# Performance work log

Hardware: AMD Instinct MI355X
Metric: run time of the kernel (lower is better)

## Reference

```python
import jax, jax.numpy as jnp
import numpy as np

# Model dims (DeepSeek-V2-Lite-like MLA)
B, S, DIM, H = 2, 2048, 2048, 16
QR, KVR = 1536, 512          # q_lora_rank, kv_lora_rank
DN, DR, DV = 128, 64, 128    # qk_nope_head_dim, qk_rope_head_dim, v_head_dim
QKD = DN + DR                # qk_head_dim = 192
SCALE = QKD ** -0.5          # max_seq_len == original_seq_len -> no mscale correction
EPS = float(jnp.finfo(jnp.float32).eps)  # torch.nn.RMSNorm default eps


def rmsnorm(x, w):
    return x * jax.lax.rsqrt(jnp.mean(x * x, axis=-1, keepdims=True) + EPS) * w


def rope(x, cos, sin):
    # x: [B, S, H, D]; cos/sin: [S, D//2]. Matches torch.view_as_complex on
    # consecutive (real, imag) pairs, multiply by freqs_cis, flatten back.
    xr, xi = x[..., 0::2], x[..., 1::2]
    c = cos[None, :, None, :]
    s = sin[None, :, None, :]
    yr = xr * c - xi * s
    yi = xr * s + xi * c
    return jnp.stack([yr, yi], axis=-1).reshape(x.shape)


def _xavier(key, out_f, in_f):
    lim = (6.0 / (in_f + out_f)) ** 0.5
    return jax.random.uniform(key, (out_f, in_f), jnp.float32, -lim, lim)


def setup_inputs() -> dict:
    key = jax.random.key(0)
    ks = jax.random.split(key, 8)
    x = jax.random.normal(ks[0], (B, S, DIM), jnp.float32)
    # rotary tables: theta=10000, rope dim = DR
    inv = 1.0 / (10000.0 ** (np.arange(0, DR, 2, dtype=np.float64) / DR))
    ang = np.arange(S, dtype=np.float64)[:, None] * inv[None, :]
    freqs_cos = jnp.asarray(np.cos(ang), jnp.float32)
    freqs_sin = jnp.asarray(np.sin(ang), jnp.float32)
    # causal mask [S, S]: 0 on/below diagonal, -1e9 above
    idx = jnp.arange(S)
    mask = jnp.where(idx[:, None] >= idx[None, :], 0.0, -1e9).astype(jnp.float32)
    return {
        "x": x,
        "freqs_cos": freqs_cos,
        "freqs_sin": freqs_sin,
        "mask": mask,
        "wq_a_w": _xavier(ks[1], QR, DIM), "wq_a_b": jnp.zeros((QR,), jnp.float32),
        "q_norm_w": jnp.ones((QR,), jnp.float32),
        "wq_b_w": _xavier(ks[2], H * QKD, QR), "wq_b_b": jnp.zeros((H * QKD,), jnp.float32),
        "wkv_a_w": _xavier(ks[3], KVR + DR, DIM), "wkv_a_b": jnp.zeros((KVR + DR,), jnp.float32),
        "kv_norm_w": jnp.ones((KVR,), jnp.float32),
        "wkv_b_w": _xavier(ks[4], H * (DN + DV), KVR), "wkv_b_b": jnp.zeros((H * (DN + DV),), jnp.float32),
        "wo_w": _xavier(ks[5], DIM, H * DV), "wo_b": jnp.zeros((DIM,), jnp.float32),
        "start_pos": 0,
    }


def reference(x, freqs_cos, freqs_sin, mask,
              wq_a_w, wq_a_b, q_norm_w, wq_b_w, wq_b_b,
              wkv_a_w, wkv_a_b, kv_norm_w, wkv_b_w, wkv_b_b,
              wo_w, wo_b, start_pos):
    bsz, seqlen, _ = x.shape
    # low-rank Q: wq_b(RMSNorm(wq_a(x)))
    q = rmsnorm(x @ wq_a_w.T + wq_a_b, q_norm_w) @ wq_b_w.T + wq_b_b
    q = q.reshape(bsz, seqlen, H, QKD)
    q_nope, q_pe = q[..., :DN], q[..., DN:]
    q_pe = rope(q_pe, freqs_cos, freqs_sin)
    # low-rank KV
    kv_a = x @ wkv_a_w.T + wkv_a_b               # [B,S,KVR+DR]
    kv_c, k_pe = kv_a[..., :KVR], kv_a[..., KVR:]
    k_pe = rope(k_pe[:, :, None, :], freqs_cos, freqs_sin)   # [B,S,1,DR]
    q = jnp.concatenate([q_nope, q_pe], axis=-1)             # [B,S,H,QKD]
    kv = rmsnorm(kv_c, kv_norm_w) @ wkv_b_w.T + wkv_b_b
    kv = kv.reshape(bsz, seqlen, H, DN + DV)
    k_nope, v = kv[..., :DN], kv[..., DN:]
    k = jnp.concatenate(
        [k_nope, jnp.broadcast_to(k_pe, (bsz, seqlen, H, DR))], axis=-1)
    scores = jnp.einsum('bshd,bthd->bsht', q, k) * SCALE
    scores = scores + mask[None, :, None, :]
    p = jax.nn.softmax(scores.astype(jnp.float32), axis=-1).astype(x.dtype)
    out = jnp.einsum('bsht,bthd->bshd', p, v).reshape(bsz, seqlen, H * DV)
    return out @ wo_w.T + wo_b
```

## Files before the change

kernel.cpp:

```cpp
#include <hip/hip_runtime.h>

#define SLEN 2048
#define NROW 4096
#define NH   16
#define SCALE_QK 0.07216878364870322f
#define RMS_EPS 1.1920928955078125e-07f

typedef __attribute__((ext_vector_type(8))) short bf16x8;
typedef __attribute__((ext_vector_type(4))) float f32x4;

__device__ __forceinline__ float b2f(short s) {
  union { float f; unsigned u; } x; x.u = ((unsigned)(unsigned short)s) << 16; return x.f;
}
__device__ __forceinline__ short f2b(float f) {
  union { float f; unsigned u; } x; x.f = f;
  unsigned r = x.u + 0x7FFFu + ((x.u >> 16) & 1u);
  return (short)(r >> 16);
}

#define GLOAD_LDS16(g, l) __builtin_amdgcn_global_load_lds( \
  (__attribute__((address_space(1))) void*)(g),             \
  (__attribute__((address_space(3))) void*)(l), 16, 0, 0)

__global__ __launch_bounds__(256) void f2b4_kernel(const float* __restrict__ in,
                                                   short* __restrict__ out, int n4) {
  int i = blockIdx.x * 256 + threadIdx.x;
  if (i >= n4) return;
  float4 v = ((const float4*)in)[i];
  short4 o = make_short4(f2b(v.x), f2b(v.y), f2b(v.z), f2b(v.w));
  ((short4*)out)[i] = o;
}

template<int OUT_BF16>
__global__ __launch_bounds__(256)
void gemm_bt_kernel(const short* __restrict__ A, const short* __restrict__ W,
                    const float* __restrict__ bias, void* __restrict__ Cout,
                    int M, int N, int K)
{
  __shared__ short sA[128 * 32];
  __shared__ short sB[128 * 32];
  int nbn = N >> 7;
  int nwg = gridDim.x;
  int wg = blockIdx.x;
  int cpx = nwg >> 3;
  wg = (wg & 7) * cpx + (wg >> 3);
  int bm = wg / nbn, bn = wg % nbn;
  int tid = threadIdx.x, wid = tid >> 6, lane = tid & 63;
  int wr = wid >> 1, wc = wid & 1;
  int lr = lane & 15, lg = lane >> 4;
  int srow = lane >> 2;
  int skk = (lane & 3) * 8;
  f32x4 acc[4][4] = {};
  const size_t baseA = (size_t)bm * 128 * K;
  const size_t baseW = (size_t)bn * 128 * K;

  for (int k0 = 0; k0 < K; k0 += 32) {
#pragma unroll
    for (int i = 0; i < 2; ++i) {
      int c = wid + i * 4;
      int r = c * 16 + srow;
      GLOAD_LDS16(A + baseA + (size_t)r * K + k0 + skk, &sA[c * 512]);
      GLOAD_LDS16(W + baseW + (size_t)r * K + k0 + skk, &sB[c * 512]);
    }
    asm volatile("s_waitcnt vmcnt(0)" ::: "memory");
    __syncthreads();
    bf16x8 av[4], bv[4];
#pragma unroll
    for (int m = 0; m < 4; ++m) av[m] = *(const bf16x8*)&sA[(wr * 64 + m * 16 + lr) * 32 + lg * 8];
#pragma unroll
    for (int n = 0; n < 4; ++n) bv[n] = *(const bf16x8*)&sB[(wc * 64 + n * 16 + lr) * 32 + lg * 8];
#pragma unroll
    for (int m = 0; m < 4; ++m)
#pragma unroll
      for (int n = 0; n < 4; ++n)
        acc[m][n] = __builtin_amdgcn_mfma_f32_16x16x32_bf16(av[m], bv[n], acc[m][n], 0, 0, 0);
    __syncthreads();
  }

  int row0 = bm * 128 + wr * 64, col0 = bn * 128 + wc * 64;
#pragma unroll
  for (int n = 0; n < 4; ++n) {
    int col = col0 + n * 16 + lr;
    float bb = bias[col];
#pragma unroll
    for (int m = 0; m < 4; ++m) {
#pragma unroll
      for (int j = 0; j < 4; ++j) {
        int row = row0 + m * 16 + lg * 4 + j;
        float v = acc[m][n][j] + bb;
        if (OUT_BF16) ((short*)Cout)[(size_t)row * N + col] = f2b(v);
        else          ((float*)Cout)[(size_t)row * N + col] = v;
      }
    }
  }
}

__global__ __launch_bounds__(256)
void norm_rope_kernel(const float* __restrict__ c1, const float* __restrict__ qw,
                      const float* __restrict__ kvw, const float* __restrict__ fcos,
                      const float* __restrict__ fsin, short* __restrict__ qan,
                      short* __restrict__ kvn, short* __restrict__ kpe)
{
  int row = blockIdx.x;
  int s = row & (SLEN - 1);
  const float* r = c1 + (size_t)row * 2176;
  int tid = threadIdx.x, wid = tid >> 6, lane = tid & 63;
  float vq[6], vk[2];
  float sq = 0.f, sk = 0.f;
#pragma unroll
  for (int i = 0; i < 6; ++i) { vq[i] = r[tid + i * 256]; sq += vq[i] * vq[i]; }
#pragma unroll
  for (int i = 0; i < 2; ++i) { vk[i] = r[1536 + tid + i * 256]; sk += vk[i] * vk[i]; }
#pragma unroll
  for (int off = 32; off > 0; off >>= 1) {
    sq += __shfl_xor(sq, off, 64);
    sk += __shfl_xor(sk, off, 64);
  }
  __shared__ float red[2][4];
  if (lane == 0) { red[0][wid] = sq; red[1][wid] = sk; }
  __syncthreads();
  sq = red[0][0] + red[0][1] + red[0][2] + red[0][3];
  sk = red[1][0] + red[1][1] + red[1][2] + red[1][3];
  float rq = rsqrtf(sq * (1.f / 1536.f) + RMS_EPS);
  float rk = rsqrtf(sk * (1.f / 512.f) + RMS_EPS);
#pragma unroll
  for (int i = 0; i < 6; ++i) qan[(size_t)row * 1536 + tid + i * 256] = f2b(vq[i] * rq * qw[tid + i * 256]);
#pragma unroll
  for (int i = 0; i < 2; ++i) kvn[(size_t)row * 512 + tid + i * 256] = f2b(vk[i] * rk * kvw[tid + i * 256]);
  if (tid < 32) {
    float xr = r[2048 + tid * 2], xi = r[2048 + tid * 2 + 1];
    float c = fcos[s * 32 + tid], sn = fsin[s * 32 + tid];
    kpe[(size_t)row * 64 + tid * 2]     = f2b(xr * c - xi * sn);
    kpe[(size_t)row * 64 + tid * 2 + 1] = f2b(xr * sn + xi * c);
  }
}

__global__ __launch_bounds__(256)
void rope_q_kernel(short* __restrict__ qf, const float* __restrict__ fcos,
                   const float* __restrict__ fsin)
{
  int idx = blockIdx.x * 256 + threadIdx.x;
  int pr = idx & 31; int h = (idx >> 5) & 15; int row = idx >> 9;
  int s = row & (SLEN - 1);
  short2* p = (short2*)(qf + (size_t)row * 3072 + h * 192 + 128 + pr * 2);
  short2 v = *p;
  float xr = b2f(v.x), xi = b2f(v.y);
  float c = fcos[s * 32 + pr], sn = fsin[s * 32 + pr];
  v.x = f2b(xr * c - xi * sn);
  v.y = f2b(xr * sn + xi * c);
  *p = v;
}

__device__ __forceinline__ void softmax16(f32x4* sacc, float p[4][4], float* m_i,
                                          float* l_i, f32x4* oacc, int t0, int srow0, int lr)
{
  float rmax[4];
#pragma unroll
  for (int j = 0; j < 4; ++j) rmax[j] = -1e30f;
#pragma unroll
  for (int tt = 0; tt < 4; ++tt) {
    int t = t0 + tt * 16 + lr;
#pragma unroll
    for (int j = 0; j < 4; ++j) {
      float x = sacc[tt][j] * SCALE_QK;
      if (t > srow0 + j) x = -1e30f;
      p[tt][j] = x;
      rmax[j] = fmaxf(rmax[j], x);
    }
  }
#pragma unroll
  for (int off = 1; off < 16; off <<= 1)
#pragma unroll
    for (int j = 0; j < 4; ++j) rmax[j] = fmaxf(rmax[j], __shfl_xor(rmax[j], off, 64));
  bool grow = false;
#pragma unroll
  for (int j = 0; j < 4; ++j) grow = grow || (rmax[j] > m_i[j] + 8.f);
  if (__any((int)grow)) {
    float sf[4];
#pragma unroll
    for (int j = 0; j < 4; ++j) {
      float mn = fmaxf(m_i[j], rmax[j]);
      sf[j] = __expf(m_i[j] - mn);
      m_i[j] = mn;
      l_i[j] *= sf[j];
    }
#pragma unroll
    for (int dt = 0; dt < 8; ++dt)
#pragma unroll
      for (int j = 0; j < 4; ++j) oacc[dt][j] *= sf[j];
  }
  float rsum[4] = {0.f, 0.f, 0.f, 0.f};
#pragma unroll
  for (int tt = 0; tt < 4; ++tt)
#pragma unroll
    for (int j = 0; j < 4; ++j) {
      float e = __expf(p[tt][j] - m_i[j]);
      p[tt][j] = e;
      rsum[j] += e;
    }
#pragma unroll
  for (int off = 1; off < 16; off <<= 1)
#pragma unroll
    for (int j = 0; j < 4; ++j) rsum[j] += __shfl_xor(rsum[j], off, 64);
#pragma unroll
  for (int j = 0; j < 4; ++j) l_i[j] += rsum[j];
}

__global__ __launch_bounds__(256, 2)
void attn_kernel(const short* __restrict__ qf, const short* __restrict__ kvf,
                 const short* __restrict__ kpe, short* __restrict__ obuf)
{
  __shared__ short sK[64 * 200];
  __shared__ short sVt[128 * 72];
  __shared__ short sPA[4][16 * 72];
  __shared__ short sPB[4][16 * 72];
  int bid = blockIdx.x;
  bid = (bid & 7) * 64 + (bid >> 3);
  int i = bid & 15, h = (bid >> 4) & 15, b = bid >> 8;
  int qtA = i, qtB = 31 - i;
  int base = b * SLEN;
  int tid = threadIdx.x, wid = tid >> 6, lane = tid & 63;
  int lr = lane & 15, lg = lane >> 4;
  int qrowA = base + qtA * 64 + wid * 16;
  int qrowB = base + qtB * 64 + wid * 16;

  bf16x8 qfragA[6], qfragB[6];
  {
    const short* qpA = qf + (size_t)(qrowA + lr) * 3072 + h * 192;
    const short* qpB = qf + (size_t)(qrowB + lr) * 3072 + h * 192;
#pragma unroll
    for (int kc = 0; kc < 6; ++kc) {
      qfragA[kc] = *(const bf16x8*)(qpA + kc * 32 + lg * 8);
      qfragB[kc] = *(const bf16x8*)(qpB + kc * 32 + lg * 8);
    }
  }
  f32x4 oaccA[8] = {}, oaccB[8] = {};
  float mA[4], lA[4], mB[4], lB[4];
#pragma unroll
  for (int j = 0; j < 4; ++j) { mA[j] = mB[j] = -1e30f; lA[j] = lB[j] = 0.f; }
  int srow0A = qtA * 64 + wid * 16 + lg * 4;
  int srow0B = qtB * 64 + wid * 16 + lg * 4;
  int str = tid >> 2, sp4 = tid & 3;
  int tpair = tid & 31, d0v = (tid >> 5) * 16;
  short* sPAw = sPA[wid];
  short* sPBw = sPB[wid];

  for (int it = 0; it <= qtB; ++it) {
    int t0 = it * 64;
    {
      const short* src = kvf + (size_t)(base + t0 + str) * 4096 + h * 256 + sp4 * 32;
      short* dst = &sK[str * 200 + sp4 * 32];
#pragma unroll
      for (int k = 0; k < 4; ++k) *(bf16x8*)(dst + k * 8) = *(const bf16x8*)(src + k * 8);
      const short* srcp = kpe + (size_t)(base + t0 + str) * 64 + sp4 * 16;
      short* dstp = &sK[str * 200 + 128 + sp4 * 16];
#pragma unroll
      for (int k = 0; k < 2; ++k) *(bf16x8*)(dstp + k * 8) = *(const bf16x8*)(srcp + k * 8);
      int tv = tpair * 2;
      const short* sv0 = kvf + (size_t)(base + t0 + tv) * 4096 + h * 256 + 128 + d0v;
      const short* sv1 = sv0 + 4096;
      bf16x8 va0 = *(const bf16x8*)(sv0);
      bf16x8 va1 = *(const bf16x8*)(sv0 + 8);
      bf16x8 vb0 = *(const bf16x8*)(sv1);
      bf16x8 vb1 = *(const bf16x8*)(sv1 + 8);
#pragma unroll
      for (int k = 0; k < 8; ++k) {
        unsigned w0 = (unsigned)(unsigned short)va0[k] | ((unsigned)(unsigned short)vb0[k] << 16);
        *((unsigned*)(sVt + (size_t)(d0v + k) * 72) + tpair) = w0;
        unsigned w1 = (unsigned)(unsigned short)va1[k] | ((unsigned)(unsigned short)vb1[k] << 16);
        *((unsigned*)(sVt + (size_t)(d0v + 8 + k) * 72) + tpair) = w1;
      }
    }
    __syncthreads();
    bool doA = (it <= qtA);

    f32x4 saccB[4] = {};
#pragma unroll
    for (int tt = 0; tt < 4; ++tt)
#pragma unroll
      for (int kc = 0; kc < 6; ++kc) {
        bf16x8 kf = *(const bf16x8*)&sK[(tt * 16 + lr) * 200 + kc * 32 + lg * 8];
        saccB[tt] = __builtin_amdgcn_mfma_f32_16x16x32_bf16(qfragB[kc], kf, saccB[tt], 0, 0, 0);
      }
    f32x4 saccA[4] = {};
    if (doA) {
#pragma unroll
      for (int tt = 0; tt < 4; ++tt)
#pragma unroll
        for (int kc = 0; kc < 6; ++kc) {
          bf16x8 kf = *(const bf16x8*)&sK[(tt * 16 + lr) * 200 + kc * 32 + lg * 8];
          saccA[tt] = __builtin_amdgcn_mfma_f32_16x16x32_bf16(qfragA[kc], kf, saccA[tt], 0, 0, 0);
        }
    }
    {
      float pB[4][4];
      softmax16(saccB, pB, mB, lB, oaccB, t0, srow0B, lr);
#pragma unroll
      for (int tt = 0; tt < 4; ++tt)
#pragma unroll
        for (int j = 0; j < 4; ++j)
          sPBw[(lg * 4 + j) * 72 + tt * 16 + lr] = f2b(pB[tt][j]);
    }
    if (doA) {
      float pA[4][4];
      softmax16(saccA, pA, mA, lA, oaccA, t0, srow0A, lr);
#pragma unroll
      for (int tt = 0; tt < 4; ++tt)
#pragma unroll
        for (int j = 0; j < 4; ++j)
          sPAw[(lg * 4 + j) * 72 + tt * 16 + lr] = f2b(pA[tt][j]);
    }
    asm volatile("s_waitcnt lgkmcnt(0)" ::: "memory");
    {
      bf16x8 pf[2];
#pragma unroll
      for (int kc = 0; kc < 2; ++kc) pf[kc] = *(const bf16x8*)&sPBw[lr * 72 + kc * 32 + lg * 8];
#pragma unroll
      for (int dt = 0; dt < 8; ++dt)
#pragma unroll
        for (int kc = 0; kc < 2; ++kc) {
          bf16x8 vf = *(const bf16x8*)&sVt[(dt * 16 + lr) * 72 + kc * 32 + lg * 8];
          oaccB[dt] = __builtin_amdgcn_mfma_f32_16x16x32_bf16(pf[kc], vf, oaccB[dt], 0, 0, 0);
        }
    }
    if (doA) {
      bf16x8 pf[2];
#pragma unroll
      for (int kc = 0; kc < 2; ++kc) pf[kc] = *(const bf16x8*)&sPAw[lr * 72 + kc * 32 + lg * 8];
#pragma unroll
      for (int dt = 0; dt < 8; ++dt)
#pragma unroll
        for (int kc = 0; kc < 2; ++kc) {
          bf16x8 vf = *(const bf16x8*)&sVt[(dt * 16 + lr) * 72 + kc * 32 + lg * 8];
          oaccA[dt] = __builtin_amdgcn_mfma_f32_16x16x32_bf16(pf[kc], vf, oaccA[dt], 0, 0, 0);
        }
    }
    __syncthreads();
  }

  float invA[4], invB[4];
#pragma unroll
  for (int j = 0; j < 4; ++j) { invA[j] = 1.f / lA[j]; invB[j] = 1.f / lB[j]; }
#pragma unroll
  for (int dt = 0; dt < 8; ++dt)
#pragma unroll
    for (int j = 0; j < 4; ++j) {
      int rowA = qrowA + lg * 4 + j;
      int rowB = qrowB + lg * 4 + j;
      obuf[(size_t)rowA * 2048 + h * 128 + dt * 16 + lr] = f2b(oaccA[dt][j] * invA[j]);
      obuf[(size_t)rowB * 2048 + h * 128 + dt * 16 + lr] = f2b(oaccB[dt][j] * invB[j]);
    }
}

extern "C" void kernel_launch(void* const* d_in, const int* in_sizes, int n_in,
                              void* d_out, int out_size, void* d_ws, size_t ws_size,
                              hipStream_t stream)
{
  const float* x    = (const float*)d_in[0];
  const float* fcos = (const float*)d_in[1];
  const float* fsin = (const float*)d_in[2];
  const float* wqa   = (const float*)d_in[4];
  const float* wqab  = (const float*)d_in[5];
  const float* qnw   = (const float*)d_in[6];
  const float* wqb   = (const float*)d_in[7];
  const float* wqbb  = (const float*)d_in[8];
  const float* wkva  = (const float*)d_in[9];
  const float* wkvab = (const float*)d_in[10];
  const float* kvnw  = (const float*)d_in[11];
  const float* wkvb  = (const float*)d_in[12];
  const float* wkvbb = (const float*)d_in[13];
  const float* wo    = (const float*)d_in[14];
  const float* wob   = (const float*)d_in[15];
  float* out = (float*)d_out;

  char* ws = (char*)d_ws;
  size_t off = 0;
  auto alloc = [&](size_t bytes) {
    char* p = ws + off;
    off += (bytes + 255) & ~(size_t)255;
    return p;
  };
  short* xb     = (short*)alloc(4096ull * 2048 * 2);
  short* w1     = (short*)alloc(2176ull * 2048 * 2);
  float* b1     = (float*)alloc(2176 * 4);
  short* wqb16  = (short*)alloc(3072ull * 1536 * 2);
  short* wkvb16 = (short*)alloc(4096ull * 512 * 2);
  short* wob16  = (short*)alloc(2048ull * 2048 * 2);
  float* c1     = (float*)alloc(4096ull * 2176 * 4);
  short* qan    = (short*)alloc(4096ull * 1536 * 2);
  short* kvn    = (short*)alloc(4096ull * 512 * 2);
  short* kpe    = (short*)alloc(4096ull * 64 * 2);
  short* qfull  = (short*)alloc(4096ull * 3072 * 2);
  short* kvfull = (short*)alloc(4096ull * 4096 * 2);
  short* obuf   = (short*)alloc(4096ull * 2048 * 2);
  (void)ws_size; (void)in_sizes; (void)n_in; (void)out_size;

  f2b4_kernel<<<8192, 256, 0, stream>>>(x, xb, 2097152);
  f2b4_kernel<<<3072, 256, 0, stream>>>(wqa, w1, 786432);
  f2b4_kernel<<<1152, 256, 0, stream>>>(wkva, w1 + 1536ull * 2048, 294912);
  hipMemsetAsync(w1 + 2112ull * 2048, 0, 64ull * 2048 * 2, stream);
  hipMemcpyAsync(b1, wqab, 1536 * 4, hipMemcpyDeviceToDevice, stream);
  hipMemcpyAsync(b1 + 1536, wkvab, 576 * 4, hipMemcpyDeviceToDevice, stream);
  hipMemsetAsync(b1 + 2112, 0, 64 * 4, stream);
  f2b4_kernel<<<4608, 256, 0, stream>>>(wqb, wqb16, 1179648);
  f2b4_kernel<<<2048, 256, 0, stream>>>(wkvb, wkvb16, 524288);
  f2b4_kernel<<<4096, 256, 0, stream>>>(wo, wob16, 1048576);

  gemm_bt_kernel<0><<<544, 256, 0, stream>>>(xb, w1, b1, c1, 4096, 2176, 2048);
  norm_rope_kernel<<<4096, 256, 0, stream>>>(c1, qnw, kvnw, fcos, fsin, qan, kvn, kpe);
  gemm_bt_kernel<1><<<768, 256, 0, stream>>>(qan, wqb16, wqbb, qfull, 4096, 3072, 1536);
  gemm_bt_kernel<1><<<1024, 256, 0, stream>>>(kvn, wkvb16, wkvbb, kvfull, 4096, 4096, 512);
  rope_q_kernel<<<8192, 256, 0, stream>>>(qfull, fcos, fsin);
  attn_kernel<<<512, 256, 0, stream>>>(qfull, kvfull, kpe, obuf);
  gemm_bt_kernel<0><<<512, 256, 0, stream>>>(obuf, wob16, wob, out, 4096, 2048, 2048);
}
```

Before: 563.6 us.

## Prefetch next K/V tile into registers, share P buffer, raise occupancy in attention

Restructures the attention loop so the next K/V tile's global loads are issued into registers after the QK MFMAs and written to LDS at the start of the next iteration, overlapping global latency with softmax and PV compute. The two per-wave P buffers are merged into one, with the key index permuted in both the P and V^T layouts so P can be stored as short4 vectors. Causal masking now runs only on the diagonal tile, s_setprio brackets the MFMA sections, and launch bounds move from 2 to 3 blocks per CU. The register prefetch and higher occupancy target compete for VGPRs and may cause spills.

```diff
diff --git a/kernel.cpp b/kernel.cpp
--- a/kernel.cpp
+++ b/kernel.cpp
@@ -152,7 +152,8 @@
 }
 
 __device__ __forceinline__ void softmax16(f32x4* sacc, float p[4][4], float* m_i,
-                                          float* l_i, f32x4* oacc, int t0, int srow0, int lr)
+                                          float* l_i, f32x4* oacc, int t0, int srow0,
+                                          int lr, bool msk)
 {
   float rmax[4];
 #pragma unroll
@@ -163,7 +164,7 @@
 #pragma unroll
     for (int j = 0; j < 4; ++j) {
       float x = sacc[tt][j] * SCALE_QK;
-      if (t > srow0 + j) x = -1e30f;
+      if (msk && (t > srow0 + j)) x = -1e30f;
       p[tt][j] = x;
       rmax[j] = fmaxf(rmax[j], x);
     }
@@ -206,14 +207,13 @@
   for (int j = 0; j < 4; ++j) l_i[j] += rsum[j];
 }
 
-__global__ __launch_bounds__(256, 2)
+__global__ __launch_bounds__(256, 3)
 void attn_kernel(const short* __restrict__ qf, const short* __restrict__ kvf,
                  const short* __restrict__ kpe, short* __restrict__ obuf)
 {
   __shared__ short sK[64 * 200];
   __shared__ short sVt[128 * 72];
-  __shared__ short sPA[4][16 * 72];
-  __shared__ short sPB[4][16 * 72];
+  __shared__ short sP[4][16 * 72];
   int bid = blockIdx.x;
   bid = (bid & 7) * 64 + (bid >> 3);
   int i = bid & 15, h = (bid >> 4) & 15, b = bid >> 8;
@@ -242,38 +242,50 @@
   int srow0B = qtB * 64 + wid * 16 + lg * 4;
   int str = tid >> 2, sp4 = tid & 3;
   int tpair = tid & 31, d0v = (tid >> 5) * 16;
-  short* sPAw = sPA[wid];
-  short* sPBw = sPB[wid];
-
+  int xv = (tpair & 15) + (tpair >> 4) * 32;
+  int tb = 4 * (tpair & 15) + 2 * (tpair >> 4);
+  short* sPw = sP[wid];
+
+  bf16x8 kr[4], per[2], va0, va1, vb0, vb1;
+  auto LOADR = [&](int it) {
+    int t0 = it * 64;
+    const short* src = kvf + (size_t)(base + t0 + str) * 4096 + h * 256 + sp4 * 32;
+#pragma unroll
+    for (int k = 0; k < 4; ++k) kr[k] = *(const bf16x8*)(src + k * 8);
+    const short* srcp = kpe + (size_t)(base + t0 + str) * 64 + sp4 * 16;
+#pragma unroll
+    for (int k = 0; k < 2; ++k) per[k] = *(const bf16x8*)(srcp + k * 8);
+    const short* sv0 = kvf + (size_t)(base + t0 + xv) * 4096 + h * 256 + 128 + d0v;
+    const short* sv1 = sv0 + (size_t)16 * 4096;
+    va0 = *(const bf16x8*)(sv0);
+    va1 = *(const bf16x8*)(sv0 + 8);
+    vb0 = *(const bf16x8*)(sv1);
+    vb1 = *(const bf16x8*)(sv1 + 8);
+  };
+  auto WRITELDS = [&]() {
+    short* dst = &sK[str * 200 + sp4 * 32];
+#pragma unroll
+    for (int k = 0; k < 4; ++k) *(bf16x8*)(dst + k * 8) = kr[k];
+    short* dstp = &sK[str * 200 + 128 + sp4 * 16];
+#pragma unroll
+    for (int k = 0; k < 2; ++k) *(bf16x8*)(dstp + k * 8) = per[k];
+#pragma unroll
+    for (int k = 0; k < 8; ++k) {
+      unsigned w0 = (unsigned)(unsigned short)va0[k] | ((unsigned)(unsigned short)vb0[k] << 16);
+      *(unsigned*)&sVt[(d0v + k) * 72 + tb] = w0;
+      unsigned w1 = (unsigned)(unsigned short)va1[k] | ((unsigned)(unsigned short)vb1[k] << 16);
+      *(unsigned*)&sVt[(d0v + 8 + k) * 72 + tb] = w1;
+    }
+  };
+
+  LOADR(0);
   for (int it = 0; it <= qtB; ++it) {
     int t0 = it * 64;
-    {
-      const short* src = kvf + (size_t)(base + t0 + str) * 4096 + h * 256 + sp4 * 32;
-      short* dst = &sK[str * 200 + sp4 * 32];
-#pragma unroll
-      for (int k = 0; k < 4; ++k) *(bf16x8*)(dst + k * 8) = *(const bf16x8*)(src + k * 8);
-      const short* srcp = kpe + (size_t)(base + t0 + str) * 64 + sp4 * 16;
-      short* dstp = &sK[str * 200 + 128 + sp4 * 16];
-#pragma unroll
-      for (int k = 0; k < 2; ++k) *(bf16x8*)(dstp + k * 8) = *(const bf16x8*)(srcp + k * 8);
-      int tv = tpair * 2;
-      const short* sv0 = kvf + (size_t)(base + t0 + tv) * 4096 + h * 256 + 128 + d0v;
-      const short* sv1 = sv0 + 4096;
-      bf16x8 va0 = *(const bf16x8*)(sv0);
-      bf16x8 va1 = *(const bf16x8*)(sv0 + 8);
-      bf16x8 vb0 = *(const bf16x8*)(sv1);
-      bf16x8 vb1 = *(const bf16x8*)(sv1 + 8);
-#pragma unroll
-      for (int k = 0; k < 8; ++k) {
-        unsigned w0 = (unsigned)(unsigned short)va0[k] | ((unsigned)(unsigned short)vb0[k] << 16);
-        *((unsigned*)(sVt + (size_t)(d0v + k) * 72) + tpair) = w0;
-        unsigned w1 = (unsigned)(unsigned short)va1[k] | ((unsigned)(unsigned short)vb1[k] << 16);
-        *((unsigned*)(sVt + (size_t)(d0v + 8 + k) * 72) + tpair) = w1;
-      }
-    }
+    WRITELDS();
     __syncthreads();
     bool doA = (it <= qtA);
 
+    __builtin_amdgcn_s_setprio(1);
     f32x4 saccB[4] = {};
 #pragma unroll
     for (int tt = 0; tt < 4; ++tt)
@@ -292,29 +304,27 @@
           saccA[tt] = __builtin_amdgcn_mfma_f32_16x16x32_bf16(qfragA[kc], kf, saccA[tt], 0, 0, 0);
         }
     }
+    __builtin_amdgcn_s_setprio(0);
+
+    if (it < qtB) LOADR(it + 1);
+
     {
       float pB[4][4];
-      softmax16(saccB, pB, mB, lB, oaccB, t0, srow0B, lr);
-#pragma unroll
-      for (int tt = 0; tt < 4; ++tt)
-#pragma unroll
-        for (int j = 0; j < 4; ++j)
-          sPBw[(lg * 4 + j) * 72 + tt * 16 + lr] = f2b(pB[tt][j]);
-    }
-    if (doA) {
-      float pA[4][4];
-      softmax16(saccA, pA, mA, lA, oaccA, t0, srow0A, lr);
-#pragma unroll
-      for (int tt = 0; tt < 4; ++tt)
-#pragma unroll
-        for (int j = 0; j < 4; ++j)
-          sPAw[(lg * 4 + j) * 72 + tt * 16 + lr] = f2b(pA[tt][j]);
-    }
-    asm volatile("s_waitcnt lgkmcnt(0)" ::: "memory");
+      softmax16(saccB, pB, mB, lB, oaccB, t0, srow0B, lr, it == qtB);
+#pragma unroll
+      for (int j = 0; j < 4; ++j) {
+        short4 w = make_short4(f2b(pB[0][j]), f2b(pB[1][j]), f2b(pB[2][j]), f2b(pB[3][j]));
+        *(short4*)&sPw[(lg * 4 + j) * 72 + lr * 4] = w;
+      }
+    }
+    float pA[4][4];
+    if (doA) softmax16(saccA, pA, mA, lA, oaccA, t0, srow0A, lr, it == qtA);
+
     {
       bf16x8 pf[2];
 #pragma unroll
-      for (int kc = 0; kc < 2; ++kc) pf[kc] = *(const bf16x8*)&sPBw[lr * 72 + kc * 32 + lg * 8];
+      for (int kc = 0; kc < 2; ++kc) pf[kc] = *(const bf16x8*)&sPw[lr * 72 + kc * 32 + lg * 8];
+      __builtin_amdgcn_s_setprio(1);
 #pragma unroll
       for (int dt = 0; dt < 8; ++dt)
 #pragma unroll
@@ -322,11 +332,18 @@
           bf16x8 vf = *(const bf16x8*)&sVt[(dt * 16 + lr) * 72 + kc * 32 + lg * 8];
           oaccB[dt] = __builtin_amdgcn_mfma_f32_16x16x32_bf16(pf[kc], vf, oaccB[dt], 0, 0, 0);
         }
+      __builtin_amdgcn_s_setprio(0);
     }
     if (doA) {
+#pragma unroll
+      for (int j = 0; j < 4; ++j) {
+        short4 w = make_short4(f2b(pA[0][j]), f2b(pA[1][j]), f2b(pA[2][j]), f2b(pA[3][j]));
+        *(short4*)&sPw[(lg * 4 + j) * 72 + lr * 4] = w;
+      }
       bf16x8 pf[2];
 #pragma unroll
-      for (int kc = 0; kc < 2; ++kc) pf[kc] = *(const bf16x8*)&sPAw[lr * 72 + kc * 32 + lg * 8];
+      for (int kc = 0; kc < 2; ++kc) pf[kc] = *(const bf16x8*)&sPw[lr * 72 + kc * 32 + lg * 8];
+      __builtin_amdgcn_s_setprio(1);
 #pragma unroll
       for (int dt = 0; dt < 8; ++dt)
 #pragma unroll
@@ -334,6 +351,7 @@
           bf16x8 vf = *(const bf16x8*)&sVt[(dt * 16 + lr) * 72 + kc * 32 + lg * 8];
           oaccA[dt] = __builtin_amdgcn_mfma_f32_16x16x32_bf16(pf[kc], vf, oaccA[dt], 0, 0, 0);
         }
+      __builtin_amdgcn_s_setprio(0);
     }
     __syncthreads();
   }
```

Measured after the change: 1.483 ms. 163% more time.
